# Kernel tuning notes

Measured on AMD Instinct MI355X. Metric: run time of the kernel, lower is better.

Reference implementation:

```python
import jax, jax.numpy as jnp
import numpy as np
from jax import lax

B, C, H, W = 8, 128, 128, 128
K = 3
RED = 8

def setup_inputs() -> dict:
    key = jax.random.key(0)
    ks = jax.random.split(key, 8)
    s = 0.05
    return {
        "x": jax.random.normal(ks[0], (B, C, H, W), dtype=jnp.float32),
        "altitude": jax.random.normal(ks[1], (B, 128), dtype=jnp.float32),
        "W1": jax.random.normal(ks[2], (128, 128), dtype=jnp.float32) * s,          # Linear(128,128), no bias
        "W2": jax.random.normal(ks[3], (128 * K * K, 128), dtype=jnp.float32) * s,  # Linear(128,128*k*k)
        "conv_w": jax.random.normal(ks[4], (C, C), dtype=jnp.float32) * s,          # 1x1 conv weight [out,in]
        "conv_b": jax.random.normal(ks[5], (C,), dtype=jnp.float32) * s,
        "ca_w1": jax.random.normal(ks[6], (C // RED, C), dtype=jnp.float32) * s,    # CA squeeze 1x1 conv
        "ca_w2": jax.random.normal(ks[7], (C, C // RED), dtype=jnp.float32) * s,    # CA excite 1x1 conv
    }

def reference(x, altitude, W1, W2, conv_w, conv_b, ca_w1, ca_w2):
    b, c, h, w = x.shape
    # kernel generator MLP: [b,128] -> [b, 128*K*K] -> (b*c, 1, K, K)
    feat = jax.nn.leaky_relu(altitude @ W1.T, negative_slope=0.1)
    kern = (feat @ W2.T).reshape(b * c, 1, K, K)
    # per-sample, per-channel conv: groups = b*c (pure generated depthwise)
    pad = (K - 1) // 2
    xr = x.reshape(1, b * c, h, w)
    out = lax.conv_general_dilated(
        xr, kern, window_strides=(1, 1), padding=[(pad, pad), (pad, pad)],
        dimension_numbers=("NCHW", "OIHW", "NCHW"), feature_group_count=b * c)
    out = jax.nn.relu(out).reshape(b, c, h, w)
    # 1x1 pointwise conv
    out = jnp.einsum("bchw,oc->bohw", out, conv_w) + conv_b[None, :, None, None]
    # channel attention from altitude
    a1 = jax.nn.leaky_relu(altitude @ ca_w1.T, negative_slope=0.1)
    att = jax.nn.sigmoid(a1 @ ca_w2.T)  # [b, c]
    return out + x * att[:, :, None, None]
```

## Files before the change

### kernel.cpp

```cpp
#include <hip/hip_runtime.h>
#include <math.h>

typedef __attribute__((ext_vector_type(8))) __bf16 bf16x8;
typedef __attribute__((ext_vector_type(4))) float f32x4;

#define PLANE 16384
#define ROWW 128


__global__ __launch_bounds__(256) void precompute_kernel(
    const float* __restrict__ altitude,
    const float* __restrict__ W1,
    const float* __restrict__ W2,
    const float* __restrict__ ca_w1,
    const float* __restrict__ ca_w2,
    const float* __restrict__ conv_w,
    float* __restrict__ ws)
{
    int bid = blockIdx.x;
    int b = bid >> 2;
    int q = bid & 3;
    int t = threadIdx.x;
    __shared__ float alt_s[128];
    __shared__ float feat_s[128];
    __shared__ float a1_s[16];

    if (t < 128) alt_s[t] = altitude[b * 128 + t];
    __syncthreads();

    if (t < 128) {
        float s = 0.f;
        const float* wrow = W1 + t * 128;
        for (int j = 0; j < 128; ++j) s += alt_s[j] * wrow[j];
        feat_s[t] = (s >= 0.f) ? s : 0.1f * s;
    } else if (t < 144 && q == 1) {
        int r = t - 128;
        float s = 0.f;
        const float* wrow = ca_w1 + r * 128;
        for (int j = 0; j < 128; ++j) s += alt_s[j] * wrow[j];
        a1_s[r] = (s >= 0.f) ? s : 0.1f * s;
    }
    __syncthreads();

    for (int i = t; i < 288; i += 256) {
        int m = q * 288 + i;
        float s = 0.f;
        const float* wrow = W2 + m * 128;
        for (int j = 0; j < 128; ++j) s += feat_s[j] * wrow[j];
        int c = m / 9, k = m % 9;
        ws[b * 1152 + k * 128 + c] = s;
    }
    if (q == 1 && t < 128) {
        float s = 0.f;
        const float* wrow = ca_w2 + t * 16;
        for (int r = 0; r < 16; ++r) s += a1_s[r] * wrow[r];
        ws[9216 + b * 128 + t] = 1.f / (1.f + expf(-s));
    }
    if (q == 2 && t < 256) {
        int kc   = t >> 6;
        int lane = t & 63;
        int o  = b * 16 + (lane & 15);
        int cb = kc * 32 + 8 * (lane >> 4);
        bf16x8 v;
        #pragma unroll
        for (int j = 0; j < 8; ++j)
            v[j] = (__bf16)conv_w[o * 128 + cb + j];
        ushort* wf = (ushort*)(ws + 10240);
        *reinterpret_cast<bf16x8*>(wf + ((size_t)(b * 4 + kc) * 64 + lane) * 8) = v;
    }
}

__global__ __launch_bounds__(256, 4) void fused_kernel(
    const float* __restrict__ x,
    const float* __restrict__ conv_b,
    const float* __restrict__ ws,
    float* __restrict__ out)
{
    const float* __restrict__ kern_w = ws;
    const float* __restrict__ att_w  = ws + 9216;
    const ushort* __restrict__ wfrag = (const ushort*)(ws + 10240);

    int bid = blockIdx.x;
    int b = bid & 7;
    int h = bid >> 3;

    __shared__ __align__(16) ushort dwT[128 * 136];
    __shared__ __align__(16) float ktaps[1152];

    int t = threadIdx.x;
    const float* __restrict__ xb = x + (size_t)b * 128 * PLANE;

    for (int i = t; i < 288; i += 256) {
        float4 v = *(const float4*)(kern_w + b * 1152 + i * 4);
        *(float4*)(&ktaps[i * 4]) = v;
    }
    __syncthreads();

    {
        int pg = t & 15;
        int cg = t >> 4;
        int gp0 = pg * 8;
        int c0 = cg * 8;

        int   rT = (h > 0)   ? h - 1 : h;
        int   rB = (h < 127) ? h + 1 : h;
        float mT = (h > 0)   ? 1.f : 0.f;
        float mB = (h < 127) ? 1.f : 0.f;
        float mL = (pg > 0)  ? 1.f : 0.f;
        float mR = (pg < 15) ? 1.f : 0.f;

        bf16x8 bv0, bv1, bv2, bv3, bv4, bv5, bv6, bv7;

#define ROWACC(A, B, KL, KC, KR) {                                     \
        float l_ = __shfl_up((B).w, 1) * mL;                           \
        float r_ = __shfl_down((A).x, 1) * mR;                         \
        o0 = fmaf((KL), l_,    fmaf((KC), (A).x, fmaf((KR), (A).y, o0))); \
        o1 = fmaf((KL), (A).x, fmaf((KC), (A).y, fmaf((KR), (A).z, o1))); \
        o2 = fmaf((KL), (A).y, fmaf((KC), (A).z, fmaf((KR), (A).w, o2))); \
        o3 = fmaf((KL), (A).z, fmaf((KC), (A).w, fmaf((KR), (B).x, o3))); \
        o4 = fmaf((KL), (A).w, fmaf((KC), (B).x, fmaf((KR), (B).y, o4))); \
        o5 = fmaf((KL), (B).x, fmaf((KC), (B).y, fmaf((KR), (B).z, o5))); \
        o6 = fmaf((KL), (B).y, fmaf((KC), (B).z, fmaf((KR), (B).w, o6))); \
        o7 = fmaf((KL), (B).z, fmaf((KC), (B).w, fmaf((KR), r_,    o7))); }

#define DW_CH(CI) {                                                    \
        const float* q_ = xb + (size_t)(c0 + (CI)) * PLANE;            \
        const float* pT = q_ + rT * ROWW + gp0;                        \
        const float* pC = q_ + h  * ROWW + gp0;                        \
        const float* pB = q_ + rB * ROWW + gp0;                        \
        float4 aT = *(const float4*)pT, bT = *(const float4*)(pT + 4); \
        float4 aC = *(const float4*)pC, bC = *(const float4*)(pC + 4); \
        float4 aB = *(const float4*)pB, bB = *(const float4*)(pB + 4); \
        const float* tp = ktaps + (c0 + (CI));                         \
        float k0 = tp[0]   * mT, k1 = tp[128] * mT, k2 = tp[256] * mT; \
        float k3 = tp[384],      k4 = tp[512],      k5 = tp[640];      \
        float k6 = tp[768] * mB, k7 = tp[896] * mB, k8 = tp[1024]* mB; \
        float o0 = 0.f, o1 = 0.f, o2 = 0.f, o3 = 0.f;                  \
        float o4 = 0.f, o5 = 0.f, o6 = 0.f, o7 = 0.f;                  \
        ROWACC(aT, bT, k0, k1, k2)                                     \
        ROWACC(aC, bC, k3, k4, k5)                                     \
        ROWACC(aB, bB, k6, k7, k8)                                     \
        bv0[(CI)] = (__bf16)fmaxf(o0, 0.f);                            \
        bv1[(CI)] = (__bf16)fmaxf(o1, 0.f);                            \
        bv2[(CI)] = (__bf16)fmaxf(o2, 0.f);                            \
        bv3[(CI)] = (__bf16)fmaxf(o3, 0.f);                            \
        bv4[(CI)] = (__bf16)fmaxf(o4, 0.f);                            \
        bv5[(CI)] = (__bf16)fmaxf(o5, 0.f);                            \
        bv6[(CI)] = (__bf16)fmaxf(o6, 0.f);                            \
        bv7[(CI)] = (__bf16)fmaxf(o7, 0.f); }

        DW_CH(0) DW_CH(1) DW_CH(2) DW_CH(3)
        DW_CH(4) DW_CH(5) DW_CH(6) DW_CH(7)
#undef DW_CH
#undef ROWACC

        int s = pg & 7;
        int chunkoff = (cg ^ s) * 8;
#define ST(J) *reinterpret_cast<bf16x8*>(&dwT[(pg * 8 + (J)) * 136 + chunkoff]) = bv##J;
        ST(0) ST(1) ST(2) ST(3) ST(4) ST(5) ST(6) ST(7)
#undef ST
    }
    __syncthreads();
    __builtin_amdgcn_sched_barrier(0);

    {
        int wid  = t >> 6;
        int lane = t & 63;
        int r = lane & 15;
        int g = lane >> 4;

        for (int ot = 0; ot < 2; ++ot) {
            int otile = wid * 2 + ot;

            bf16x8 bfr[4];
            #pragma unroll
            for (int kc = 0; kc < 4; ++kc)
                bfr[kc] = *reinterpret_cast<const bf16x8*>(
                    wfrag + ((size_t)(otile * 4 + kc) * 64 + lane) * 8);

            f32x4 acc[8];
            #pragma unroll
            for (int pt = 0; pt < 8; ++pt) acc[pt] = (f32x4){0.f, 0.f, 0.f, 0.f};

            #pragma unroll
            for (int pt = 0; pt < 8; ++pt) {
                int px = pt * 16 + r;
                int srow = px * 136;
                int s2 = (px >> 3) & 7;
                #pragma unroll
                for (int kc = 0; kc < 4; ++kc) {
                    bf16x8 a = *reinterpret_cast<const bf16x8*>(
                        &dwT[srow + (((kc * 4 + g) ^ s2) * 8)]);
                    acc[pt] = __builtin_amdgcn_mfma_f32_16x16x32_bf16(a, bfr[kc], acc[pt], 0, 0, 0);
                }
            }

            int o = otile * 16 + r;
            float bi = conv_b[o];
            float at = att_w[b * 128 + o];
            size_t rowoff = (size_t)(b * 128 + o) * PLANE + (size_t)h * ROWW;
            const float* xrow = x + rowoff;
            float* orow = out + rowoff;
            #pragma unroll
            for (int pt = 0; pt < 8; ++pt) {
                int px = pt * 16 + g * 4;
                float4 xv = *(const float4*)(xrow + px);
                float4 ov;
                ov.x = acc[pt][0] + bi + xv.x * at;
                ov.y = acc[pt][1] + bi + xv.y * at;
                ov.z = acc[pt][2] + bi + xv.z * at;
                ov.w = acc[pt][3] + bi + xv.w * at;
                *(float4*)(orow + px) = ov;
            }
        }
    }
}

extern "C" void kernel_launch(void* const* d_in, const int* in_sizes, int n_in,
                              void* d_out, int out_size, void* d_ws, size_t ws_size,
                              hipStream_t stream) {
    (void)in_sizes; (void)n_in; (void)out_size; (void)ws_size;
    const float* x        = (const float*)d_in[0];
    const float* altitude = (const float*)d_in[1];
    const float* W1       = (const float*)d_in[2];
    const float* W2       = (const float*)d_in[3];
    const float* conv_w   = (const float*)d_in[4];
    const float* conv_b   = (const float*)d_in[5];
    const float* ca_w1    = (const float*)d_in[6];
    const float* ca_w2    = (const float*)d_in[7];
    float* out = (float*)d_out;
    float* ws  = (float*)d_ws;

    hipLaunchKernelGGL(precompute_kernel, dim3(32), dim3(256), 0, stream,
                       altitude, W1, W2, ca_w1, ca_w2, conv_w, ws);
    hipLaunchKernelGGL(fused_kernel, dim3(1024), dim3(256), 0, stream,
                       x, conv_b, ws, out);
}
```

Measured before the change: 47.06 us.

## Double block size to 512 threads, halving per-thread depthwise and MFMA work

```diff
diff --git a/kernel.cpp b/kernel.cpp
--- a/kernel.cpp
+++ b/kernel.cpp
@@ -2,6 +2,7 @@
 #include <math.h>
 
 typedef __attribute__((ext_vector_type(8))) __bf16 bf16x8;
+typedef __attribute__((ext_vector_type(4))) __bf16 bf16x4;
 typedef __attribute__((ext_vector_type(4))) float f32x4;
 
 #define PLANE 16384
@@ -48,13 +49,13 @@
         const float* wrow = W2 + m * 128;
         for (int j = 0; j < 128; ++j) s += feat_s[j] * wrow[j];
         int c = m / 9, k = m % 9;
-        ws[b * 1152 + k * 128 + c] = s;
+        ws[b * 1536 + c * 12 + k] = s;
     }
     if (q == 1 && t < 128) {
         float s = 0.f;
         const float* wrow = ca_w2 + t * 16;
         for (int r = 0; r < 16; ++r) s += a1_s[r] * wrow[r];
-        ws[9216 + b * 128 + t] = 1.f / (1.f + expf(-s));
+        ws[12288 + b * 128 + t] = 1.f / (1.f + expf(-s));
     }
     if (q == 2 && t < 256) {
         int kc   = t >> 6;
@@ -65,33 +66,33 @@
         #pragma unroll
         for (int j = 0; j < 8; ++j)
             v[j] = (__bf16)conv_w[o * 128 + cb + j];
-        ushort* wf = (ushort*)(ws + 10240);
+        ushort* wf = (ushort*)(ws + 13312);
         *reinterpret_cast<bf16x8*>(wf + ((size_t)(b * 4 + kc) * 64 + lane) * 8) = v;
     }
 }
 
-__global__ __launch_bounds__(256, 4) void fused_kernel(
+__global__ __launch_bounds__(512, 8) void fused_kernel(
     const float* __restrict__ x,
     const float* __restrict__ conv_b,
     const float* __restrict__ ws,
     float* __restrict__ out)
 {
     const float* __restrict__ kern_w = ws;
-    const float* __restrict__ att_w  = ws + 9216;
-    const ushort* __restrict__ wfrag = (const ushort*)(ws + 10240);
+    const float* __restrict__ att_w  = ws + 12288;
+    const ushort* __restrict__ wfrag = (const ushort*)(ws + 13312);
 
     int bid = blockIdx.x;
     int b = bid & 7;
     int h = bid >> 3;
 
     __shared__ __align__(16) ushort dwT[128 * 136];
-    __shared__ __align__(16) float ktaps[1152];
+    __shared__ __align__(16) float ktaps[128 * 12];
 
     int t = threadIdx.x;
     const float* __restrict__ xb = x + (size_t)b * 128 * PLANE;
 
-    for (int i = t; i < 288; i += 256) {
-        float4 v = *(const float4*)(kern_w + b * 1152 + i * 4);
+    for (int i = t; i < 384; i += 512) {
+        float4 v = *(const float4*)(kern_w + b * 1536 + i * 4);
         *(float4*)(&ktaps[i * 4]) = v;
     }
     __syncthreads();
@@ -100,7 +101,7 @@
         int pg = t & 15;
         int cg = t >> 4;
         int gp0 = pg * 8;
-        int c0 = cg * 8;
+        int c0 = cg * 4;
 
         int   rT = (h > 0)   ? h - 1 : h;
         int   rB = (h < 127) ? h + 1 : h;
@@ -109,7 +110,7 @@
         float mL = (pg > 0)  ? 1.f : 0.f;
         float mR = (pg < 15) ? 1.f : 0.f;
 
-        bf16x8 bv0, bv1, bv2, bv3, bv4, bv5, bv6, bv7;
+        bf16x4 bv0, bv1, bv2, bv3, bv4, bv5, bv6, bv7;
 
 #define ROWACC(A, B, KL, KC, KR) {                                     \
         float l_ = __shfl_up((B).w, 1) * mL;                           \
@@ -131,10 +132,13 @@
         float4 aT = *(const float4*)pT, bT = *(const float4*)(pT + 4); \
         float4 aC = *(const float4*)pC, bC = *(const float4*)(pC + 4); \
         float4 aB = *(const float4*)pB, bB = *(const float4*)(pB + 4); \
-        const float* tp = ktaps + (c0 + (CI));                         \
-        float k0 = tp[0]   * mT, k1 = tp[128] * mT, k2 = tp[256] * mT; \
-        float k3 = tp[384],      k4 = tp[512],      k5 = tp[640];      \
-        float k6 = tp[768] * mB, k7 = tp[896] * mB, k8 = tp[1024]* mB; \
+        const float* tp = ktaps + (c0 + (CI)) * 12;                    \
+        float4 kA = *(const float4*)tp;                                \
+        float4 kB = *(const float4*)(tp + 4);                          \
+        float  k8v = tp[8];                                            \
+        float k0 = kA.x * mT, k1 = kA.y * mT, k2 = kA.z * mT;          \
+        float k3 = kA.w,      k4 = kB.x,      k5 = kB.y;               \
+        float k6 = kB.z * mB, k7 = kB.w * mB, k8 = k8v * mB;           \
         float o0 = 0.f, o1 = 0.f, o2 = 0.f, o3 = 0.f;                  \
         float o4 = 0.f, o5 = 0.f, o6 = 0.f, o7 = 0.f;                  \
         ROWACC(aT, bT, k0, k1, k2)                                     \
@@ -150,13 +154,11 @@
         bv7[(CI)] = (__bf16)fmaxf(o7, 0.f); }
 
         DW_CH(0) DW_CH(1) DW_CH(2) DW_CH(3)
-        DW_CH(4) DW_CH(5) DW_CH(6) DW_CH(7)
 #undef DW_CH
 #undef ROWACC
 
-        int s = pg & 7;
-        int chunkoff = (cg ^ s) * 8;
-#define ST(J) *reinterpret_cast<bf16x8*>(&dwT[(pg * 8 + (J)) * 136 + chunkoff]) = bv##J;
+        int slotoff = (((cg >> 1) ^ pg) * 8) + ((cg & 1) * 4);
+#define ST(J) *reinterpret_cast<bf16x4*>(&dwT[(pg * 8 + (J)) * 136 + slotoff]) = bv##J;
         ST(0) ST(1) ST(2) ST(3) ST(4) ST(5) ST(6) ST(7)
 #undef ST
     }
@@ -164,54 +166,50 @@
     __builtin_amdgcn_sched_barrier(0);
 
     {
-        int wid  = t >> 6;
+        int w    = t >> 6;
         int lane = t & 63;
         int r = lane & 15;
         int g = lane >> 4;
 
-        for (int ot = 0; ot < 2; ++ot) {
-            int otile = wid * 2 + ot;
-
-            bf16x8 bfr[4];
+        bf16x8 bfr[4];
+        #pragma unroll
+        for (int kc = 0; kc < 4; ++kc)
+            bfr[kc] = *reinterpret_cast<const bf16x8*>(
+                wfrag + ((size_t)(w * 4 + kc) * 64 + lane) * 8);
+
+        f32x4 acc[8];
+        #pragma unroll
+        for (int pt = 0; pt < 8; ++pt) acc[pt] = (f32x4){0.f, 0.f, 0.f, 0.f};
+
+        #pragma unroll
+        for (int pt = 0; pt < 8; ++pt) {
+            int px = pt * 16 + r;
+            int srow = px * 136;
+            int s2 = px >> 3;
             #pragma unroll
-            for (int kc = 0; kc < 4; ++kc)
-                bfr[kc] = *reinterpret_cast<const bf16x8*>(
-                    wfrag + ((size_t)(otile * 4 + kc) * 64 + lane) * 8);
-
-            f32x4 acc[8];
-            #pragma unroll
-            for (int pt = 0; pt < 8; ++pt) acc[pt] = (f32x4){0.f, 0.f, 0.f, 0.f};
-
-            #pragma unroll
-            for (int pt = 0; pt < 8; ++pt) {
-                int px = pt * 16 + r;
-                int srow = px * 136;
-                int s2 = (px >> 3) & 7;
-                #pragma unroll
-                for (int kc = 0; kc < 4; ++kc) {
-                    bf16x8 a = *reinterpret_cast<const bf16x8*>(
-                        &dwT[srow + (((kc * 4 + g) ^ s2) * 8)]);
-                    acc[pt] = __builtin_amdgcn_mfma_f32_16x16x32_bf16(a, bfr[kc], acc[pt], 0, 0, 0);
-                }
+            for (int kc = 0; kc < 4; ++kc) {
+                bf16x8 a = *reinterpret_cast<const bf16x8*>(
+                    &dwT[srow + (((kc * 4 + g) ^ s2) * 8)]);
+                acc[pt] = __builtin_amdgcn_mfma_f32_16x16x32_bf16(a, bfr[kc], acc[pt], 0, 0, 0);
             }
-
-            int o = otile * 16 + r;
-            float bi = conv_b[o];
-            float at = att_w[b * 128 + o];
-            size_t rowoff = (size_t)(b * 128 + o) * PLANE + (size_t)h * ROWW;
-            const float* xrow = x + rowoff;
-            float* orow = out + rowoff;
-            #pragma unroll
-            for (int pt = 0; pt < 8; ++pt) {
-                int px = pt * 16 + g * 4;
-                float4 xv = *(const float4*)(xrow + px);
-                float4 ov;
-                ov.x = acc[pt][0] + bi + xv.x * at;
-                ov.y = acc[pt][1] + bi + xv.y * at;
-                ov.z = acc[pt][2] + bi + xv.z * at;
-                ov.w = acc[pt][3] + bi + xv.w * at;
-                *(float4*)(orow + px) = ov;
-            }
+        }
+
+        int o = w * 16 + r;
+        float bi = conv_b[o];
+        float at = att_w[b * 128 + o];
+        size_t rowoff = (size_t)(b * 128 + o) * PLANE + (size_t)h * ROWW;
+        const float* xrow = x + rowoff;
+        float* orow = out + rowoff;
+        #pragma unroll
+        for (int pt = 0; pt < 8; ++pt) {
+            int px = pt * 16 + g * 4;
+            float4 xv = *(const float4*)(xrow + px);
+            float4 ov;
+            ov.x = acc[pt][0] + bi + xv.x * at;
+            ov.y = acc[pt][1] + bi + xv.y * at;
+            ov.z = acc[pt][2] + bi + xv.z * at;
+            ov.w = acc[pt][3] + bi + xv.w * at;
+            *(float4*)(orow + px) = ov;
         }
     }
 }
@@ -233,6 +231,6 @@
 
     hipLaunchKernelGGL(precompute_kernel, dim3(32), dim3(256), 0, stream,
                        altitude, W1, W2, ca_w1, ca_w2, conv_w, ws);
-    hipLaunchKernelGGL(fused_kernel, dim3(1024), dim3(256), 0, stream,
+    hipLaunchKernelGGL(fused_kernel, dim3(1024), dim3(512), 0, stream,
                        x, conv_b, ws, out);
 }
```

Measured after the change: 48.77 us. 1.04x slower.
